# Kernel tuning notes

Measured on AMD Instinct MI355X. Metric: run time of the kernel, lower is better.

The kernel has to match this reference:

```python
import jax, jax.numpy as jnp
import numpy as np

B, T, N, H = 16, 49, 64, 128  # batch, input_window_size-1, nbones, hidden_size


def setup_inputs() -> dict:
    key = jax.random.key(0)
    ks = jax.random.split(key, 13)
    s = 0.1  # keep gate preactivations in a sane range
    inp = {
        "h": jax.random.normal(ks[0], (B, T, N, H), jnp.float32),
        "c_h": jax.random.normal(ks[1], (B, T, N, H), jnp.float32),
        "p": jax.random.normal(ks[2], (B, T, N, H), jnp.float32),
        "g_t": jax.random.normal(ks[3], (B, T, 1, H), jnp.float32),
        "c_g_t": jax.random.normal(ks[4], (B, T, 1, H), jnp.float32),
        # 8 h-update gates stacked: order = (i, f_lt, f_ft, f_rt, f_s, g, o, c)
        "U": jax.random.normal(ks[5], (8, T, H, H), jnp.float32) * s,     # acts on p
        "Wt": jax.random.normal(ks[6], (8, T, 3 * H, H), jnp.float32) * s,  # acts on [h_before,h,h_after]
        "Ws": jax.random.normal(ks[7], (8, T, H, H), jnp.float32) * s,    # acts on h_s_before
        "Zt": jax.random.normal(ks[8], (8, T, H, H), jnp.float32) * s,    # acts on g_t
        "b": jax.random.normal(ks[9], (8, T, 1, H), jnp.float32) * s,
        # 3 g_t-update gates stacked: order = (forget_f, g, o)
        "Wg": jax.random.normal(ks[10], (3, T, H, H), jnp.float32) * s,
        "Zg": jax.random.normal(ks[11], (3, T, H, H), jnp.float32) * s,
        "bg": jax.random.normal(ks[12], (3, T, 1, H), jnp.float32) * s,
        "train": 0,
    }
    return inp


def _forward(h, c_h, p, g_t, c_g_t, U, Wt, Ws, Zt, b, Wg, Zg, bg):
    zt = jnp.zeros_like(h[:, :1])        # temporal padding [B,1,N,H]
    zs = jnp.zeros_like(h[:, :, :1])     # spatial  padding [B,T,1,H]
    h_tb = jnp.concatenate([zt, h[:, :-1]], axis=1)
    h_ta = jnp.concatenate([h[:, 1:], zt], axis=1)
    h_tba = jnp.concatenate([h_tb, h, h_ta], axis=3)   # [B,T,N,3H]
    c_tb = jnp.concatenate([zt, c_h[:, :-1]], axis=1)
    c_ta = jnp.concatenate([c_h[:, 1:], zt], axis=1)
    h_sb = jnp.concatenate([zs, h[:, :, :-1]], axis=2)
    c_sb = jnp.concatenate([zs, c_h[:, :, :-1]], axis=2)

    # all 8 gate preactivations at once; per-timestep weights contracted with einsum
    pre = (jnp.einsum('btnh,gthk->gbtnk', p, U)
           + jnp.einsum('btnd,gtdk->gbtnk', h_tba, Wt)
           + jnp.einsum('btnh,gthk->gbtnk', h_sb, Ws)
           + jnp.einsum('btoh,gthk->gbtok', g_t, Zt)   # o == 1, broadcasts over bones
           + b[:, None])                               # [8,B,T,N,H]
    i_n, f_lt, f_ft, f_rt, f_s, g_n, o_n = jax.nn.sigmoid(pre[:7])
    c_n = jnp.tanh(pre[7])

    c_h_new = (i_n * c_n + f_lt * c_tb + f_ft * c_h + f_rt * c_ta
               + f_s * c_sb + g_n * c_g_t)
    h_new = o_n * jnp.tanh(c_h_new)

    # global (g_t) state update
    h_mean = jnp.mean(h_new, axis=2, keepdims=True)    # [B,T,1,H]
    f_gtf = jax.nn.sigmoid(jnp.einsum('btnh,thk->btnk', h_new, Wg[0])
                           + jnp.einsum('btoh,thk->btok', g_t, Zg[0]) + bg[0])
    g_gtg = jax.nn.sigmoid(jnp.einsum('btoh,thk->btok', h_mean, Wg[1])
                           + jnp.einsum('btoh,thk->btok', g_t, Zg[1]) + bg[1])
    o_gto = jax.nn.sigmoid(jnp.einsum('btoh,thk->btok', h_mean, Wg[2])
                           + jnp.einsum('btoh,thk->btok', g_t, Zg[2]) + bg[2])
    c_g_new = jnp.mean(f_gtf * c_h_new, axis=2, keepdims=True) + g_gtg * c_g_t
    g_new = jnp.tanh(c_g_new) * o_gto
    return h_new, c_h_new, g_new, c_g_new


def reference(h, c_h, p, g_t, c_g_t, U, Wt, Ws, Zt, b, Wg, Zg, bg, train):
    return _forward(h, c_h, p, g_t, c_g_t, U, Wt, Ws, Zt, b, Wg, Zg, bg)
```

## Files before the change

kernel.cpp:

```cpp
#include <hip/hip_runtime.h>
#include <hip/hip_bf16.h>

#define TD 49
#define BD 16
#define ND 64
#define HD 128

typedef float  f32x4  __attribute__((ext_vector_type(4)));
typedef __bf16 bf16x8 __attribute__((ext_vector_type(8)));
typedef __bf16 bf16x4 __attribute__((ext_vector_type(4)));

#define WP_OFF   0u
#define HB_OFF   38535168u
#define ACT_ELEMS 6422528u
#define PB_OFF   44957696u
#define GB_OFF   51380224u
#define GT_ELEMS 100352u
#define ZP_OFF   51480576u

#define OUT_H    0
#define OUT_CH   6422528
#define OUT_G    12845056
#define OUT_CG   12945408

#define KPAD 136
#define LDS1_BYTES 65536
#define LDS2_BYTES 118784

__device__ __forceinline__ float sigf(float x) {
    return 1.0f / (1.0f + exp2f(-1.442695041f * x));
}
__device__ __forceinline__ float tanhf_fast(float x) {
    x = fminf(fmaxf(x, -20.f), 20.f);
    float e = exp2f(2.885390082f * x);
    return (e - 1.f) / (e + 1.f);
}
__device__ __forceinline__ void gload16(const void* g, void* l) {
    __builtin_amdgcn_global_load_lds((const __attribute__((address_space(1))) void*)g,
                                     (__attribute__((address_space(3))) void*)l, 16, 0, 0);
}

__global__ void prep_acts(const float* __restrict__ h, const float* __restrict__ p,
                          const float* __restrict__ g, __bf16* __restrict__ ws)
{
    unsigned i = blockIdx.x * 256u + threadIdx.x;
    const unsigned HU = ACT_ELEMS / 4u, GU = GT_ELEMS / 4u;
    const float* src;
    unsigned dst;
    if (i < HU)                 { src = h + (size_t)i * 4;          dst = HB_OFF + i * 4; }
    else if (i < 2u*HU)         { unsigned j = i - HU;   src = p + (size_t)j * 4; dst = PB_OFF + j * 4; }
    else if (i < 2u*HU + GU)    { unsigned j = i - 2u*HU; src = g + (size_t)j * 4; dst = GB_OFF + j * 4; }
    else if (i < 2u*HU + GU + 512u) {
        unsigned j = i - 2u*HU - GU;
        bf16x4 z = {};
        *(bf16x4*)(ws + ZP_OFF + j * 4) = z;
        return;
    } else return;
    f32x4 v = *(const f32x4*)src;
    bf16x4 w;
    w[0] = (__bf16)v[0]; w[1] = (__bf16)v[1]; w[2] = (__bf16)v[2]; w[3] = (__bf16)v[3];
    *(bf16x4*)(ws + dst) = w;
}

__global__ __launch_bounds__(256) void prep_w(
    const float* __restrict__ U, const float* __restrict__ Wt,
    const float* __restrict__ Ws, const float* __restrict__ Zt,
    __bf16* __restrict__ wp)
{
    __shared__ __bf16 tile[64 * 132];
    int bid = blockIdx.x;
    int tg  = bid / 12;
    int c   = bid % 12;
    int t   = tg >> 3, g = tg & 7;
    int gt  = g * TD + t;
    int tid = threadIdx.x;
    int k0  = c * 64;

#pragma unroll
    for (int u = 0; u < 8; ++u) {
        int unit = u * 256 + tid;
        int kk = unit >> 5;
        int h4 = (unit & 31) << 2;
        int k  = k0 + kk;
        const float* src;
        if (k < 128)      src = U  + ((size_t)(gt * 128 + k)       << 7);
        else if (k < 512) src = Wt + ((size_t)(gt * 384 + (k-128)) << 7);
        else if (k < 640) src = Ws + ((size_t)(gt * 128 + (k-512)) << 7);
        else              src = Zt + ((size_t)(gt * 128 + (k-640)) << 7);
        f32x4 v = *(const f32x4*)(src + h4);
        bf16x4 w;
        w[0] = (__bf16)v[0]; w[1] = (__bf16)v[1]; w[2] = (__bf16)v[2]; w[3] = (__bf16)v[3];
        *(bf16x4*)(tile + kk * 132 + h4) = w;
    }
    __syncthreads();
#pragma unroll
    for (int u = 0; u < 2; ++u) {
        int unit = u * 256 + tid;
        int hh = unit >> 2;
        int kg = unit & 3;
        bf16x8 v0, v1;
#pragma unroll
        for (int j = 0; j < 8; ++j) v0[j] = tile[(kg * 16 + j) * 132 + hh];
#pragma unroll
        for (int j = 0; j < 8; ++j) v1[j] = tile[(kg * 16 + 8 + j) * 132 + hh];
        __bf16* dst = wp + (size_t)(tg * 128 + hh) * 768 + k0 + kg * 16;
        *(bf16x8*)dst       = v0;
        *(bf16x8*)(dst + 8) = v1;
    }
}

__global__ __launch_bounds__(256, 2) void phase1_kernel(
    const __bf16* __restrict__ ws,
    const float* __restrict__ c_h, const float* __restrict__ c_g_t,
    const float* __restrict__ bias, float* __restrict__ out)
{
    extern __shared__ __bf16 smem[];
    const __bf16* hb = ws + HB_OFF;
    const __bf16* pb = ws + PB_OFF;
    const __bf16* gb = ws + GB_OFF;
    const __bf16* wp = ws + WP_OFF;
    const __bf16* zp = ws + ZP_OFF;

    int bid = blockIdx.x;
    int swz = (bid & 7) * 392 + (bid >> 3);
    int t     = swz >> 6;
    int rem   = swz & 63;
    int mtile = rem >> 3, ntile = rem & 7;

    int tid  = threadIdx.x;
    int wave = tid >> 6, lane = tid & 63;
    int lg = lane >> 4, l16 = lane & 15;

    const __bf16* pA[2][6];
    const __bf16* pB[2];
    int dstA[2], dstB[2];
#pragma unroll
    for (int it = 0; it < 2; ++it) {
        int chunk = it * 256 + tid;
        int row   = chunk >> 2;
        int k16   = chunk & 3;
        int ke    = (k16 ^ ((row >> 1) & 3)) * 8;
        int b_ = mtile * 2 + (row >> 6), n_ = row & 63, bt_ = b_ * TD + t;
        pA[it][0] = pb + ((bt_ * ND + n_) << 7) + ke;
        pA[it][1] = (t > 0)      ? hb + (((bt_ - 1) * ND + n_) << 7) + ke : zp + ke;
        pA[it][2] = hb + ((bt_ * ND + n_) << 7) + ke;
        pA[it][3] = (t < TD - 1) ? hb + (((bt_ + 1) * ND + n_) << 7) + ke : zp + ke;
        pA[it][4] = (n_ > 0)     ? hb + ((bt_ * ND + n_ - 1) << 7) + ke : zp + ke;
        pA[it][5] = gb + (bt_ << 7) + ke;
        int g_ = row >> 4, hc = row & 15;
        pB[it] = wp + (size_t)((t * 8 + g_) * 128 + ntile * 16 + hc) * 768 + ke;
        dstA[it] = chunk * 8;
        dstB[it] = 16384 + chunk * 8;
    }

    int rbA[2], rbB[8];
#pragma unroll
    for (int mi = 0; mi < 2; ++mi) {
        int row = wave * 32 + mi * 16 + l16;
        rbA[mi] = row * 64 + ((lg ^ ((row >> 1) & 3)) << 4);
    }
#pragma unroll
    for (int g = 0; g < 8; ++g) {
        int row = g * 16 + l16;
        rbB[g] = 32768 + row * 64 + ((lg ^ ((row >> 1) & 3)) << 4);
    }

    f32x4 acc[2][8];
    const f32x4 vzero = {0.f, 0.f, 0.f, 0.f};
#pragma unroll
    for (int mi = 0; mi < 2; ++mi)
#pragma unroll
        for (int g = 0; g < 8; ++g) acc[mi][g] = vzero;

#define STAGE(KS) do {                                                          \
        _Pragma("unroll")                                                       \
        for (int it = 0; it < 2; ++it) {                                        \
            gload16(pA[it][(KS) >> 2] + ((KS) & 3) * 32,                        \
                    smem + ((KS) & 3) * 4096 + dstA[it]);                       \
            gload16(pB[it] + (KS) * 32,                                         \
                    smem + ((KS) & 3) * 4096 + dstB[it]);                       \
        }                                                                       \
    } while (0)

    STAGE(0); STAGE(1); STAGE(2);
    asm volatile("s_waitcnt vmcnt(8)" ::: "memory");
    __builtin_amdgcn_s_barrier();

#pragma unroll
    for (int ks = 0; ks < 24; ++ks) {
        if (ks + 3 < 24) STAGE(ks + 3);
        const char* base = (const char*)smem + (ks & 3) * 8192;
        bf16x8 af[2], bfr[8];
        af[0] = *(const bf16x8*)(base + rbA[0]);
        af[1] = *(const bf16x8*)(base + rbA[1]);
#pragma unroll
        for (int g = 0; g < 8; ++g)
            bfr[g] = *(const bf16x8*)(base + rbB[g]);
#pragma unroll
        for (int g = 0; g < 8; ++g) {
            acc[0][g] = __builtin_amdgcn_mfma_f32_16x16x32_bf16(af[0], bfr[g], acc[0][g], 0, 0, 0);
            acc[1][g] = __builtin_amdgcn_mfma_f32_16x16x32_bf16(af[1], bfr[g], acc[1][g], 0, 0, 0);
        }
        if (ks < 23) {
            if (ks < 21)       asm volatile("s_waitcnt vmcnt(8)" ::: "memory");
            else if (ks == 21) asm volatile("s_waitcnt vmcnt(4)" ::: "memory");
            else               asm volatile("s_waitcnt vmcnt(0)" ::: "memory");
            __builtin_amdgcn_s_barrier();
        }
    }
#undef STAGE

    const int hcol = ntile * 16 + l16;
    float bv[8];
#pragma unroll
    for (int g = 0; g < 8; ++g) bv[g] = bias[(g * TD + t) * HD + hcol];

#pragma unroll
    for (int mi = 0; mi < 2; ++mi) {
#pragma unroll
        for (int r = 0; r < 4; ++r) {
            int RG = mtile * 128 + wave * 32 + mi * 16 + lg * 4 + r;
            int b  = RG >> 6, nn = RG & 63;
            int bt = b * TD + t;
            int base = ((bt * ND + nn) << 7) + hcol;
            float pre[8];
#pragma unroll
            for (int g = 0; g < 8; ++g) pre[g] = acc[mi][g][r] + bv[g];
            float i_  = sigf(pre[0]);
            float flt = sigf(pre[1]);
            float fft = sigf(pre[2]);
            float frt = sigf(pre[3]);
            float fs  = sigf(pre[4]);
            float gn  = sigf(pre[5]);
            float on  = sigf(pre[6]);
            float cn  = tanhf_fast(pre[7]);
            float ccur = c_h[base];
            float ctb  = (t > 0)      ? c_h[base - ND * HD] : 0.f;
            float cta  = (t < TD - 1) ? c_h[base + ND * HD] : 0.f;
            float csb  = (nn > 0)     ? c_h[base - HD]      : 0.f;
            float cg   = c_g_t[(bt << 7) + hcol];
            float cnew = i_ * cn + flt * ctb + fft * ccur + frt * cta + fs * csb + gn * cg;
            float hnew = on * tanhf_fast(cnew);
            out[OUT_H  + base] = hnew;
            out[OUT_CH + base] = cnew;
        }
    }
}

__global__ __launch_bounds__(256, 1) void phase2_kernel(
    const float* __restrict__ g_t, const float* __restrict__ c_g_t,
    const float* __restrict__ Wg,  const float* __restrict__ Zg,
    const float* __restrict__ bg,  float* __restrict__ out)
{
    extern __shared__ char sm2[];
    __bf16* A2  = (__bf16*)sm2;
    __bf16* Wb  = (__bf16*)(sm2 + 69632);
    float*  gts = (float*)(sm2 + 69632 + 34816);
    float*  hm  = (float*)(sm2 + 69632 + 34816 + 2048);
    float*  dts = (float*)(sm2 + 69632 + 34816 + 4096);

    int bid = blockIdx.x;
    int t = bid >> 2, bq = bid & 3;
    int tid = threadIdx.x;
    int wv = tid >> 6, lane = tid & 63, lg = lane >> 4, l16 = lane & 15;

    const float* hn  = out + OUT_H;
    const float* chn = out + OUT_CH;

#pragma unroll
    for (int j = 0; j < 32; ++j) {
        int fid = j * 256 + tid;
        int r = fid >> 5, k = (fid & 31) << 2;
        int b = bq * 4 + (r >> 6), n = r & 63, bt = b * TD + t;
        f32x4 v = *(const f32x4*)(hn + ((bt * ND + n) << 7) + k);
        bf16x4 w;
        w[0] = (__bf16)v[0]; w[1] = (__bf16)v[1]; w[2] = (__bf16)v[2]; w[3] = (__bf16)v[3];
        *(bf16x4*)(A2 + r * KPAD + k) = w;
    }
#pragma unroll
    for (int j = 0; j < 2; ++j) {
        int idx = j * 256 + tid;
        int b4 = idx >> 7, c = idx & 127;
        gts[idx] = g_t[(((bq * 4 + b4) * TD + t) << 7) + c];
    }
    __syncthreads();

#pragma unroll
    for (int j = 0; j < 2; ++j) {
        int idx = j * 256 + tid;
        int b4 = idx >> 7, c = idx & 127;
        float s = 0.f;
        for (int n = 0; n < 64; ++n) s += (float)A2[(b4 * 64 + n) * KPAD + c];
        hm[idx] = s * (1.f / 64.f);
    }
    __syncthreads();

    for (int m = 0; m < 5; ++m) {
        const float* M = (m < 3) ? (Zg + ((size_t)(m * TD + t) << 14))
                                 : (Wg + ((size_t)((m - 2) * TD + t) << 14));
#pragma unroll
        for (int j = 0; j < 16; ++j) {
            int fid = j * 256 + tid;
            int k = fid >> 5, c4 = (fid & 31) << 2;
            f32x4 v = *(const f32x4*)(M + (k << 7) + c4);
            bf16x4 w;
            w[0] = (__bf16)v[0]; w[1] = (__bf16)v[1]; w[2] = (__bf16)v[2]; w[3] = (__bf16)v[3];
            *(bf16x4*)(Wb + k * KPAD + c4) = w;
        }
        __syncthreads();
        const float* vec = (m >= 3) ? hm : gts;
#pragma unroll
        for (int j = 0; j < 2; ++j) {
            int idx = j * 256 + tid;
            int b4 = idx >> 7, c = idx & 127;
            float s = 0.f;
            for (int k = 0; k < 128; ++k) s += vec[b4 * 128 + k] * (float)Wb[k * KPAD + c];
            dts[(m * 4 + b4) * 128 + c] = s;
        }
        __syncthreads();
    }

    {
        const float* M = Wg + ((size_t)t << 14);
#pragma unroll
        for (int j = 0; j < 16; ++j) {
            int fid = j * 256 + tid;
            int k = fid >> 5, q = fid & 31;
            f32x4 v = *(const f32x4*)(M + (k << 7) + q * 4);
            int cb = q * 4;
            Wb[(cb + 0) * KPAD + k] = (__bf16)v[0];
            Wb[(cb + 1) * KPAD + k] = (__bf16)v[1];
            Wb[(cb + 2) * KPAD + k] = (__bf16)v[2];
            Wb[(cb + 3) * KPAD + k] = (__bf16)v[3];
        }
        __syncthreads();
    }

    f32x4 acc[4][8];
    const f32x4 vzero = {0.f, 0.f, 0.f, 0.f};
#pragma unroll
    for (int mi = 0; mi < 4; ++mi)
#pragma unroll
        for (int ni = 0; ni < 8; ++ni) acc[mi][ni] = vzero;
#pragma unroll
    for (int ks = 0; ks < 4; ++ks) {
        int kb = ks * 32 + lg * 8;
        bf16x8 a[4];
#pragma unroll
        for (int mi = 0; mi < 4; ++mi)
            a[mi] = *(const bf16x8*)(A2 + (wv * 64 + mi * 16 + l16) * KPAD + kb);
#pragma unroll
        for (int ni = 0; ni < 8; ++ni) {
            bf16x8 bfr = *(const bf16x8*)(Wb + (ni * 16 + l16) * KPAD + kb);
#pragma unroll
            for (int mi = 0; mi < 4; ++mi)
                acc[mi][ni] = __builtin_amdgcn_mfma_f32_16x16x32_bf16(a[mi], bfr, acc[mi][ni], 0, 0, 0);
        }
    }

    int b = bq * 4 + wv, bt = b * TD + t;
#pragma unroll
    for (int ni = 0; ni < 8; ++ni) {
        int col = ni * 16 + l16;
        float z = dts[(0 * 4 + wv) * 128 + col] + bg[t * HD + col];
        float macc = 0.f;
#pragma unroll
        for (int mi = 0; mi < 4; ++mi) {
#pragma unroll
            for (int r = 0; r < 4; ++r) {
                int row = mi * 16 + lg * 4 + r;
                float f  = sigf(acc[mi][ni][r] + z);
                float cv = chn[((bt * ND + row) << 7) + col];
                macc += f * cv;
            }
        }
        macc += __shfl_xor(macc, 16, 64);
        macc += __shfl_xor(macc, 32, 64);
        if (lg == 0) {
            float Mn  = macc * (1.f / 64.f);
            float g_g = sigf(dts[(3 * 4 + wv) * 128 + col] + dts[(1 * 4 + wv) * 128 + col]
                             + bg[(TD + t) * HD + col]);
            float o_g = sigf(dts[(4 * 4 + wv) * 128 + col] + dts[(2 * 4 + wv) * 128 + col]
                             + bg[(2 * TD + t) * HD + col]);
            float cgt = c_g_t[(bt << 7) + col];
            float cgn = Mn + g_g * cgt;
            out[OUT_G  + (bt << 7) + col] = tanhf_fast(cgn) * o_g;
            out[OUT_CG + (bt << 7) + col] = cgn;
        }
    }
}

extern "C" void kernel_launch(void* const* d_in, const int* in_sizes, int n_in,
                              void* d_out, int out_size, void* d_ws, size_t ws_size,
                              hipStream_t stream) {
    const float* h     = (const float*)d_in[0];
    const float* c_h   = (const float*)d_in[1];
    const float* p     = (const float*)d_in[2];
    const float* g_t   = (const float*)d_in[3];
    const float* c_g_t = (const float*)d_in[4];
    const float* U     = (const float*)d_in[5];
    const float* Wt    = (const float*)d_in[6];
    const float* Ws    = (const float*)d_in[7];
    const float* Zt    = (const float*)d_in[8];
    const float* b     = (const float*)d_in[9];
    const float* Wg    = (const float*)d_in[10];
    const float* Zg    = (const float*)d_in[11];
    const float* bg    = (const float*)d_in[12];
    float* out = (float*)d_out;
    __bf16* ws = (__bf16*)d_ws;

    prep_acts<<<12644, 256, 0, stream>>>(h, p, g_t, ws);
    prep_w<<<TD * 8 * 12, 256, 0, stream>>>(U, Wt, Ws, Zt, ws + WP_OFF);

    (void)hipFuncSetAttribute(reinterpret_cast<const void*>(phase1_kernel),
                              hipFuncAttributeMaxDynamicSharedMemorySize, LDS1_BYTES);
    (void)hipFuncSetAttribute(reinterpret_cast<const void*>(phase2_kernel),
                              hipFuncAttributeMaxDynamicSharedMemorySize, LDS2_BYTES);
    phase1_kernel<<<TD * 64, 256, LDS1_BYTES, stream>>>(ws, c_h, c_g_t, b, out);
    phase2_kernel<<<TD * 4, 256, LDS2_BYTES, stream>>>(g_t, c_g_t, Wg, Zg, bg, out);
}
```

Baseline: 234.9 us.

## Double phase1 M-tile to 256 rows with 3-stage LDS pipeline

Phase1 now computes a 256x128 output tile per block instead of 128x128, so each B-weight fragment read from LDS feeds four MFMAs rather than two, and half as many blocks are launched. The LDS ring shrinks from four stages to three with separate A and B regions, and address computation switches to 32-bit offsets. This roughly halves redundant weight traffic per output, at the cost of twice the accumulator registers (which may lower occupancy) and fewer blocks to spread across CUs.

Result: slower. 282.4 us (+20.2%).

```diff
diff --git a/kernel.cpp b/kernel.cpp
--- a/kernel.cpp
+++ b/kernel.cpp
@@ -24,7 +24,7 @@
 #define OUT_CG   12945408
 
 #define KPAD 136
-#define LDS1_BYTES 65536
+#define LDS1_BYTES 73728
 #define LDS2_BYTES 118784
 
 __device__ __forceinline__ float sigf(float x) {
@@ -115,96 +115,100 @@
     const float* __restrict__ bias, float* __restrict__ out)
 {
     extern __shared__ __bf16 smem[];
-    const __bf16* hb = ws + HB_OFF;
-    const __bf16* pb = ws + PB_OFF;
-    const __bf16* gb = ws + GB_OFF;
-    const __bf16* wp = ws + WP_OFF;
-    const __bf16* zp = ws + ZP_OFF;
 
     int bid = blockIdx.x;
-    int swz = (bid & 7) * 392 + (bid >> 3);
-    int t     = swz >> 6;
-    int rem   = swz & 63;
+    int swz = (bid & 7) * 196 + (bid >> 3);
+    int t     = swz >> 5;
+    int rem   = swz & 31;
     int mtile = rem >> 3, ntile = rem & 7;
 
     int tid  = threadIdx.x;
     int wave = tid >> 6, lane = tid & 63;
     int lg = lane >> 4, l16 = lane & 15;
 
-    const __bf16* pA[2][6];
-    const __bf16* pB[2];
-    int dstA[2], dstB[2];
+    const int n    = tid >> 2;
+    const unsigned kesw = (((tid & 3) ^ ((tid >> 3) & 3)) << 3);
+    const bool okT0 = (t > 0), okT1 = (t < TD - 1), okN = (n > 0);
+    const unsigned zoff = ZP_OFF + kesw;
+    const int tid8 = tid * 8;
+
+    unsigned rowoff[4], goff[4], offB[2];
+#pragma unroll
+    for (int it = 0; it < 4; ++it) {
+        unsigned bt_ = (unsigned)((mtile * 4 + it) * TD + t);
+        rowoff[it] = bt_ * 8192u + (unsigned)(n << 7) + kesw;
+        goff[it]   = bt_ * 128u + kesw;
+    }
 #pragma unroll
     for (int it = 0; it < 2; ++it) {
-        int chunk = it * 256 + tid;
-        int row   = chunk >> 2;
-        int k16   = chunk & 3;
-        int ke    = (k16 ^ ((row >> 1) & 3)) * 8;
-        int b_ = mtile * 2 + (row >> 6), n_ = row & 63, bt_ = b_ * TD + t;
-        pA[it][0] = pb + ((bt_ * ND + n_) << 7) + ke;
-        pA[it][1] = (t > 0)      ? hb + (((bt_ - 1) * ND + n_) << 7) + ke : zp + ke;
-        pA[it][2] = hb + ((bt_ * ND + n_) << 7) + ke;
-        pA[it][3] = (t < TD - 1) ? hb + (((bt_ + 1) * ND + n_) << 7) + ke : zp + ke;
-        pA[it][4] = (n_ > 0)     ? hb + ((bt_ * ND + n_ - 1) << 7) + ke : zp + ke;
-        pA[it][5] = gb + (bt_ << 7) + ke;
+        int row = it * 64 + n;
         int g_ = row >> 4, hc = row & 15;
-        pB[it] = wp + (size_t)((t * 8 + g_) * 128 + ntile * 16 + hc) * 768 + ke;
-        dstA[it] = chunk * 8;
-        dstB[it] = 16384 + chunk * 8;
-    }
-
-    int rbA[2], rbB[8];
-#pragma unroll
-    for (int mi = 0; mi < 2; ++mi) {
-        int row = wave * 32 + mi * 16 + l16;
+        offB[it] = WP_OFF + (unsigned)((t * 8 + g_) * 128 + ntile * 16 + hc) * 768u + kesw;
+    }
+
+    f32x4 acc[4][8];
+    const f32x4 vzero = {0.f, 0.f, 0.f, 0.f};
+#pragma unroll
+    for (int mi = 0; mi < 4; ++mi)
+#pragma unroll
+        for (int g = 0; g < 8; ++g) acc[mi][g] = vzero;
+
+    int rbA[4], rbB[8];
+#pragma unroll
+    for (int mi = 0; mi < 4; ++mi) {
+        int row = wave * 64 + mi * 16 + l16;
         rbA[mi] = row * 64 + ((lg ^ ((row >> 1) & 3)) << 4);
     }
 #pragma unroll
     for (int g = 0; g < 8; ++g) {
         int row = g * 16 + l16;
-        rbB[g] = 32768 + row * 64 + ((lg ^ ((row >> 1) & 3)) << 4);
-    }
-
-    f32x4 acc[2][8];
-    const f32x4 vzero = {0.f, 0.f, 0.f, 0.f};
-#pragma unroll
-    for (int mi = 0; mi < 2; ++mi)
-#pragma unroll
-        for (int g = 0; g < 8; ++g) acc[mi][g] = vzero;
+        rbB[g] = row * 64 + ((lg ^ ((row >> 1) & 3)) << 4);
+    }
 
 #define STAGE(KS) do {                                                          \
+        const int s_ = (KS) >> 2;                                               \
+        const int sl = (KS) % 3;                                                \
         _Pragma("unroll")                                                       \
-        for (int it = 0; it < 2; ++it) {                                        \
-            gload16(pA[it][(KS) >> 2] + ((KS) & 3) * 32,                        \
-                    smem + ((KS) & 3) * 4096 + dstA[it]);                       \
-            gload16(pB[it] + (KS) * 32,                                         \
-                    smem + ((KS) & 3) * 4096 + dstB[it]);                       \
+        for (int it = 0; it < 4; ++it) {                                        \
+            unsigned off;                                                       \
+            if (s_ == 0)      off = PB_OFF + rowoff[it];                        \
+            else if (s_ == 1) off = okT0 ? HB_OFF + rowoff[it] - 8192u : zoff;  \
+            else if (s_ == 2) off = HB_OFF + rowoff[it];                        \
+            else if (s_ == 3) off = okT1 ? HB_OFF + rowoff[it] + 8192u : zoff;  \
+            else if (s_ == 4) off = okN  ? HB_OFF + rowoff[it] - 128u  : zoff;  \
+            else              off = GB_OFF + goff[it];                          \
+            gload16(ws + off + ((KS) & 3) * 32, smem + sl * 8192 + tid8 + it * 2048); \
         }                                                                       \
+        _Pragma("unroll")                                                       \
+        for (int it = 0; it < 2; ++it)                                          \
+            gload16(ws + offB[it] + (KS) * 32,                                  \
+                    smem + 24576 + sl * 4096 + tid8 + it * 2048);               \
     } while (0)
 
-    STAGE(0); STAGE(1); STAGE(2);
-    asm volatile("s_waitcnt vmcnt(8)" ::: "memory");
+    STAGE(0); STAGE(1);
+    asm volatile("s_waitcnt vmcnt(6)" ::: "memory");
     __builtin_amdgcn_s_barrier();
 
 #pragma unroll
     for (int ks = 0; ks < 24; ++ks) {
-        if (ks + 3 < 24) STAGE(ks + 3);
-        const char* base = (const char*)smem + (ks & 3) * 8192;
-        bf16x8 af[2], bfr[8];
-        af[0] = *(const bf16x8*)(base + rbA[0]);
-        af[1] = *(const bf16x8*)(base + rbA[1]);
+        if (ks + 2 < 24) STAGE(ks + 2);
+        const char* Ab = (const char*)smem + (ks % 3) * 16384;
+        const char* Bb = (const char*)smem + 49152 + (ks % 3) * 8192;
+        bf16x8 af[4], bfr[8];
+#pragma unroll
+        for (int mi = 0; mi < 4; ++mi)
+            af[mi] = *(const bf16x8*)(Ab + rbA[mi]);
 #pragma unroll
         for (int g = 0; g < 8; ++g)
-            bfr[g] = *(const bf16x8*)(base + rbB[g]);
-#pragma unroll
-        for (int g = 0; g < 8; ++g) {
-            acc[0][g] = __builtin_amdgcn_mfma_f32_16x16x32_bf16(af[0], bfr[g], acc[0][g], 0, 0, 0);
-            acc[1][g] = __builtin_amdgcn_mfma_f32_16x16x32_bf16(af[1], bfr[g], acc[1][g], 0, 0, 0);
-        }
+            bfr[g] = *(const bf16x8*)(Bb + rbB[g]);
+#pragma unroll
+        for (int g = 0; g < 8; ++g)
+#pragma unroll
+            for (int mi = 0; mi < 4; ++mi)
+                acc[mi][g] = __builtin_amdgcn_mfma_f32_16x16x32_bf16(af[mi], bfr[g], acc[mi][g], 0, 0, 0);
         if (ks < 23) {
-            if (ks < 21)       asm volatile("s_waitcnt vmcnt(8)" ::: "memory");
-            else if (ks == 21) asm volatile("s_waitcnt vmcnt(4)" ::: "memory");
-            else               asm volatile("s_waitcnt vmcnt(0)" ::: "memory");
+            if (ks < 22) asm volatile("s_waitcnt vmcnt(6)" ::: "memory");
+            else         asm volatile("s_waitcnt vmcnt(0)" ::: "memory");
             __builtin_amdgcn_s_barrier();
         }
     }
@@ -216,10 +220,10 @@
     for (int g = 0; g < 8; ++g) bv[g] = bias[(g * TD + t) * HD + hcol];
 
 #pragma unroll
-    for (int mi = 0; mi < 2; ++mi) {
+    for (int mi = 0; mi < 4; ++mi) {
 #pragma unroll
         for (int r = 0; r < 4; ++r) {
-            int RG = mtile * 128 + wave * 32 + mi * 16 + lg * 4 + r;
+            int RG = mtile * 256 + wave * 64 + mi * 16 + lg * 4 + r;
             int b  = RG >> 6, nn = RG & 63;
             int bt = b * TD + t;
             int base = ((bt * ND + nn) << 7) + hcol;
@@ -271,8 +275,8 @@
     for (int j = 0; j < 32; ++j) {
         int fid = j * 256 + tid;
         int r = fid >> 5, k = (fid & 31) << 2;
-        int b = bq * 4 + (r >> 6), n = r & 63, bt = b * TD + t;
-        f32x4 v = *(const f32x4*)(hn + ((bt * ND + n) << 7) + k);
+        int b = bq * 4 + (r >> 6), nn = r & 63, bt = b * TD + t;
+        f32x4 v = *(const f32x4*)(hn + ((bt * ND + nn) << 7) + k);
         bf16x4 w;
         w[0] = (__bf16)v[0]; w[1] = (__bf16)v[1]; w[2] = (__bf16)v[2]; w[3] = (__bf16)v[3];
         *(bf16x4*)(A2 + r * KPAD + k) = w;
@@ -290,7 +294,7 @@
         int idx = j * 256 + tid;
         int b4 = idx >> 7, c = idx & 127;
         float s = 0.f;
-        for (int n = 0; n < 64; ++n) s += (float)A2[(b4 * 64 + n) * KPAD + c];
+        for (int nn = 0; nn < 64; ++nn) s += (float)A2[(b4 * 64 + nn) * KPAD + c];
         hm[idx] = s * (1.f / 64.f);
     }
     __syncthreads();
@@ -416,6 +420,6 @@
                               hipFuncAttributeMaxDynamicSharedMemorySize, LDS1_BYTES);
     (void)hipFuncSetAttribute(reinterpret_cast<const void*>(phase2_kernel),
                               hipFuncAttributeMaxDynamicSharedMemorySize, LDS2_BYTES);
-    phase1_kernel<<<TD * 64, 256, LDS1_BYTES, stream>>>(ws, c_h, c_g_t, b, out);
+    phase1_kernel<<<TD * 32, 256, LDS1_BYTES, stream>>>(ws, c_h, c_g_t, b, out);
     phase2_kernel<<<TD * 4, 256, LDS2_BYTES, stream>>>(g_t, c_g_t, Wg, Zg, bg, out);
 }
```

## Precompute g_t·Zt plus bias per (b,t) and drop Zt from main GEMM

Applied to the files above, without the earlier changes.

The g_t term is constant across the 64 bones, so its projection through Zt plus the bias is precomputed once per (batch, timestep, gate) in a new prep block group and added in the epilogue. The main MFMA GEMM K dimension shrinks from 768 to 640, cutting weight packing, loads and MFMA work by about a sixth. The two prep kernels are also merged into one launch. The trade-off is an extra fp32 scalar prep stage and per-element gathered loads of the precomputed term in the phase1 epilogue.

After: 282.2 us. 1.2x slower.

```diff
diff --git a/kernel.cpp b/kernel.cpp
--- a/kernel.cpp
+++ b/kernel.cpp
@@ -11,12 +11,13 @@
 typedef __bf16 bf16x4 __attribute__((ext_vector_type(4)));
 
 #define WP_OFF   0u
-#define HB_OFF   38535168u
+#define HB_OFF   32112640u
 #define ACT_ELEMS 6422528u
-#define PB_OFF   44957696u
-#define GB_OFF   51380224u
+#define PB_OFF   38535168u
+#define GB_OFF   44957696u
 #define GT_ELEMS 100352u
-#define ZP_OFF   51480576u
+#define ZP_OFF   45058048u
+#define ZB_OFF   45060096u
 
 #define OUT_H    0
 #define OUT_CH   6422528
@@ -27,6 +28,10 @@
 #define LDS1_BYTES 65536
 #define LDS2_BYTES 118784
 
+#define NB_ACTS 12644
+#define NB_W    3920
+#define NB_ZB   392
+
 __device__ __forceinline__ float sigf(float x) {
     return 1.0f / (1.0f + exp2f(-1.442695041f * x));
 }
@@ -40,86 +45,112 @@
                                      (__attribute__((address_space(3))) void*)l, 16, 0, 0);
 }
 
-__global__ void prep_acts(const float* __restrict__ h, const float* __restrict__ p,
-                          const float* __restrict__ g, __bf16* __restrict__ ws)
-{
-    unsigned i = blockIdx.x * 256u + threadIdx.x;
-    const unsigned HU = ACT_ELEMS / 4u, GU = GT_ELEMS / 4u;
-    const float* src;
-    unsigned dst;
-    if (i < HU)                 { src = h + (size_t)i * 4;          dst = HB_OFF + i * 4; }
-    else if (i < 2u*HU)         { unsigned j = i - HU;   src = p + (size_t)j * 4; dst = PB_OFF + j * 4; }
-    else if (i < 2u*HU + GU)    { unsigned j = i - 2u*HU; src = g + (size_t)j * 4; dst = GB_OFF + j * 4; }
-    else if (i < 2u*HU + GU + 512u) {
-        unsigned j = i - 2u*HU - GU;
-        bf16x4 z = {};
-        *(bf16x4*)(ws + ZP_OFF + j * 4) = z;
-        return;
-    } else return;
-    f32x4 v = *(const f32x4*)src;
-    bf16x4 w;
-    w[0] = (__bf16)v[0]; w[1] = (__bf16)v[1]; w[2] = (__bf16)v[2]; w[3] = (__bf16)v[3];
-    *(bf16x4*)(ws + dst) = w;
-}
-
-__global__ __launch_bounds__(256) void prep_w(
-    const float* __restrict__ U, const float* __restrict__ Wt,
-    const float* __restrict__ Ws, const float* __restrict__ Zt,
-    __bf16* __restrict__ wp)
+__global__ __launch_bounds__(256) void prep_kernel(
+    const float* __restrict__ h,  const float* __restrict__ p,
+    const float* __restrict__ g,  const float* __restrict__ U,
+    const float* __restrict__ Wt, const float* __restrict__ Ws,
+    const float* __restrict__ Zt, const float* __restrict__ bias,
+    __bf16* __restrict__ ws)
 {
     __shared__ __bf16 tile[64 * 132];
-    int bid = blockIdx.x;
-    int tg  = bid / 12;
-    int c   = bid % 12;
-    int t   = tg >> 3, g = tg & 7;
-    int gt  = g * TD + t;
-    int tid = threadIdx.x;
-    int k0  = c * 64;
-
-#pragma unroll
-    for (int u = 0; u < 8; ++u) {
-        int unit = u * 256 + tid;
-        int kk = unit >> 5;
-        int h4 = (unit & 31) << 2;
-        int k  = k0 + kk;
+    const int bid = blockIdx.x;
+    const int tid = threadIdx.x;
+
+    if (bid < NB_ACTS) {
+        unsigned i = bid * 256u + tid;
+        const unsigned HU = ACT_ELEMS / 4u, GU = GT_ELEMS / 4u;
         const float* src;
-        if (k < 128)      src = U  + ((size_t)(gt * 128 + k)       << 7);
-        else if (k < 512) src = Wt + ((size_t)(gt * 384 + (k-128)) << 7);
-        else if (k < 640) src = Ws + ((size_t)(gt * 128 + (k-512)) << 7);
-        else              src = Zt + ((size_t)(gt * 128 + (k-640)) << 7);
-        f32x4 v = *(const f32x4*)(src + h4);
+        unsigned dst;
+        if (i < HU)              { src = h + (size_t)i * 4;            dst = HB_OFF + i * 4; }
+        else if (i < 2u*HU)      { unsigned j = i - HU;    src = p + (size_t)j * 4; dst = PB_OFF + j * 4; }
+        else if (i < 2u*HU + GU) { unsigned j = i - 2u*HU; src = g + (size_t)j * 4; dst = GB_OFF + j * 4; }
+        else if (i < 2u*HU + GU + 512u) {
+            unsigned j = i - 2u*HU - GU;
+            bf16x4 z = {};
+            *(bf16x4*)(ws + ZP_OFF + j * 4) = z;
+            return;
+        } else return;
+        f32x4 v = *(const f32x4*)src;
         bf16x4 w;
         w[0] = (__bf16)v[0]; w[1] = (__bf16)v[1]; w[2] = (__bf16)v[2]; w[3] = (__bf16)v[3];
-        *(bf16x4*)(tile + kk * 132 + h4) = w;
-    }
-    __syncthreads();
-#pragma unroll
-    for (int u = 0; u < 2; ++u) {
-        int unit = u * 256 + tid;
-        int hh = unit >> 2;
-        int kg = unit & 3;
-        bf16x8 v0, v1;
-#pragma unroll
-        for (int j = 0; j < 8; ++j) v0[j] = tile[(kg * 16 + j) * 132 + hh];
-#pragma unroll
-        for (int j = 0; j < 8; ++j) v1[j] = tile[(kg * 16 + 8 + j) * 132 + hh];
-        __bf16* dst = wp + (size_t)(tg * 128 + hh) * 768 + k0 + kg * 16;
-        *(bf16x8*)dst       = v0;
-        *(bf16x8*)(dst + 8) = v1;
+        *(bf16x4*)(ws + dst) = w;
+        return;
+    }
+
+    if (bid < NB_ACTS + NB_W) {
+        int wb = bid - NB_ACTS;
+        int tg = wb / 10, c = wb % 10;
+        int t  = tg >> 3, gg = tg & 7;
+        int gt = gg * TD + t;
+        int k0 = c * 64;
+#pragma unroll
+        for (int u = 0; u < 8; ++u) {
+            int unit = u * 256 + tid;
+            int kk = unit >> 5;
+            int h4 = (unit & 31) << 2;
+            int k  = k0 + kk;
+            const float* src;
+            if (k < 128)      src = U  + ((size_t)(gt * 128 + k)       << 7);
+            else if (k < 512) src = Wt + ((size_t)(gt * 384 + (k-128)) << 7);
+            else              src = Ws + ((size_t)(gt * 128 + (k-512)) << 7);
+            f32x4 v = *(const f32x4*)(src + h4);
+            bf16x4 w;
+            w[0] = (__bf16)v[0]; w[1] = (__bf16)v[1]; w[2] = (__bf16)v[2]; w[3] = (__bf16)v[3];
+            *(bf16x4*)(tile + kk * 132 + h4) = w;
+        }
+        __syncthreads();
+#pragma unroll
+        for (int u = 0; u < 2; ++u) {
+            int unit = u * 256 + tid;
+            int hh = unit >> 2;
+            int kg = unit & 3;
+            bf16x8 v0, v1;
+#pragma unroll
+            for (int j = 0; j < 8; ++j) v0[j] = tile[(kg * 16 + j) * 132 + hh];
+#pragma unroll
+            for (int j = 0; j < 8; ++j) v1[j] = tile[(kg * 16 + 8 + j) * 132 + hh];
+            __bf16* dst = ws + WP_OFF + (size_t)(tg * 128 + hh) * 640 + k0 + kg * 16;
+            *(bf16x8*)dst       = v0;
+            *(bf16x8*)(dst + 8) = v1;
+        }
+        return;
+    }
+
+    {
+        int zid = bid - NB_ACTS - NB_W;
+        int t = zid >> 3, gg = zid & 7;
+        int h_ = tid & 127, bh = tid >> 7;
+        float* zbf = (float*)(ws + ZB_OFF);
+        float s[8];
+        float bv = bias[(gg * TD + t) * HD + h_];
+#pragma unroll
+        for (int b8 = 0; b8 < 8; ++b8) s[b8] = bv;
+        const float* Zrow = Zt + ((size_t)(gg * TD + t) << 14) + h_;
+        for (int k = 0; k < 128; ++k) {
+            float zv = Zrow[k << 7];
+#pragma unroll
+            for (int b8 = 0; b8 < 8; ++b8)
+                s[b8] += g[(((bh * 8 + b8) * TD + t) << 7) + k] * zv;
+        }
+#pragma unroll
+        for (int b8 = 0; b8 < 8; ++b8) {
+            int bt = (bh * 8 + b8) * TD + t;
+            zbf[(bt * 8 + gg) * HD + h_] = s[b8];
+        }
     }
 }
 
 __global__ __launch_bounds__(256, 2) void phase1_kernel(
     const __bf16* __restrict__ ws,
     const float* __restrict__ c_h, const float* __restrict__ c_g_t,
-    const float* __restrict__ bias, float* __restrict__ out)
+    float* __restrict__ out)
 {
     extern __shared__ __bf16 smem[];
     const __bf16* hb = ws + HB_OFF;
     const __bf16* pb = ws + PB_OFF;
-    const __bf16* gb = ws + GB_OFF;
     const __bf16* wp = ws + WP_OFF;
     const __bf16* zp = ws + ZP_OFF;
+    const float*  zb = (const float*)(ws + ZB_OFF);
 
     int bid = blockIdx.x;
     int swz = (bid & 7) * 392 + (bid >> 3);
@@ -131,7 +162,7 @@
     int wave = tid >> 6, lane = tid & 63;
     int lg = lane >> 4, l16 = lane & 15;
 
-    const __bf16* pA[2][6];
+    const __bf16* pA[2][5];
     const __bf16* pB[2];
     int dstA[2], dstB[2];
 #pragma unroll
@@ -146,9 +177,8 @@
         pA[it][2] = hb + ((bt_ * ND + n_) << 7) + ke;
         pA[it][3] = (t < TD - 1) ? hb + (((bt_ + 1) * ND + n_) << 7) + ke : zp + ke;
         pA[it][4] = (n_ > 0)     ? hb + ((bt_ * ND + n_ - 1) << 7) + ke : zp + ke;
-        pA[it][5] = gb + (bt_ << 7) + ke;
         int g_ = row >> 4, hc = row & 15;
-        pB[it] = wp + (size_t)((t * 8 + g_) * 128 + ntile * 16 + hc) * 768 + ke;
+        pB[it] = wp + (size_t)((t * 8 + g_) * 128 + ntile * 16 + hc) * 640 + ke;
         dstA[it] = chunk * 8;
         dstB[it] = 16384 + chunk * 8;
     }
@@ -187,8 +217,8 @@
     __builtin_amdgcn_s_barrier();
 
 #pragma unroll
-    for (int ks = 0; ks < 24; ++ks) {
-        if (ks + 3 < 24) STAGE(ks + 3);
+    for (int ks = 0; ks < 20; ++ks) {
+        if (ks + 3 < 20) STAGE(ks + 3);
         const char* base = (const char*)smem + (ks & 3) * 8192;
         bf16x8 af[2], bfr[8];
         af[0] = *(const bf16x8*)(base + rbA[0]);
@@ -201,9 +231,9 @@
             acc[0][g] = __builtin_amdgcn_mfma_f32_16x16x32_bf16(af[0], bfr[g], acc[0][g], 0, 0, 0);
             acc[1][g] = __builtin_amdgcn_mfma_f32_16x16x32_bf16(af[1], bfr[g], acc[1][g], 0, 0, 0);
         }
-        if (ks < 23) {
-            if (ks < 21)       asm volatile("s_waitcnt vmcnt(8)" ::: "memory");
-            else if (ks == 21) asm volatile("s_waitcnt vmcnt(4)" ::: "memory");
+        if (ks < 19) {
+            if (ks < 17)       asm volatile("s_waitcnt vmcnt(8)" ::: "memory");
+            else if (ks == 17) asm volatile("s_waitcnt vmcnt(4)" ::: "memory");
             else               asm volatile("s_waitcnt vmcnt(0)" ::: "memory");
             __builtin_amdgcn_s_barrier();
         }
@@ -211,10 +241,6 @@
 #undef STAGE
 
     const int hcol = ntile * 16 + l16;
-    float bv[8];
-#pragma unroll
-    for (int g = 0; g < 8; ++g) bv[g] = bias[(g * TD + t) * HD + hcol];
-
 #pragma unroll
     for (int mi = 0; mi < 2; ++mi) {
 #pragma unroll
@@ -223,9 +249,10 @@
             int b  = RG >> 6, nn = RG & 63;
             int bt = b * TD + t;
             int base = ((bt * ND + nn) << 7) + hcol;
+            const float* zrow = zb + (bt * 8) * HD + hcol;
             float pre[8];
 #pragma unroll
-            for (int g = 0; g < 8; ++g) pre[g] = acc[mi][g][r] + bv[g];
+            for (int g = 0; g < 8; ++g) pre[g] = acc[mi][g][r] + zrow[g * HD];
             float i_  = sigf(pre[0]);
             float flt = sigf(pre[1]);
             float fft = sigf(pre[2]);
@@ -271,8 +298,8 @@
     for (int j = 0; j < 32; ++j) {
         int fid = j * 256 + tid;
         int r = fid >> 5, k = (fid & 31) << 2;
-        int b = bq * 4 + (r >> 6), n = r & 63, bt = b * TD + t;
-        f32x4 v = *(const f32x4*)(hn + ((bt * ND + n) << 7) + k);
+        int b = bq * 4 + (r >> 6), nn = r & 63, bt = b * TD + t;
+        f32x4 v = *(const f32x4*)(hn + ((bt * ND + nn) << 7) + k);
         bf16x4 w;
         w[0] = (__bf16)v[0]; w[1] = (__bf16)v[1]; w[2] = (__bf16)v[2]; w[3] = (__bf16)v[3];
         *(bf16x4*)(A2 + r * KPAD + k) = w;
@@ -290,7 +317,7 @@
         int idx = j * 256 + tid;
         int b4 = idx >> 7, c = idx & 127;
         float s = 0.f;
-        for (int n = 0; n < 64; ++n) s += (float)A2[(b4 * 64 + n) * KPAD + c];
+        for (int nn = 0; nn < 64; ++nn) s += (float)A2[(b4 * 64 + nn) * KPAD + c];
         hm[idx] = s * (1.f / 64.f);
     }
     __syncthreads();
@@ -409,13 +436,12 @@
     float* out = (float*)d_out;
     __bf16* ws = (__bf16*)d_ws;
 
-    prep_acts<<<12644, 256, 0, stream>>>(h, p, g_t, ws);
-    prep_w<<<TD * 8 * 12, 256, 0, stream>>>(U, Wt, Ws, Zt, ws + WP_OFF);
+    prep_kernel<<<NB_ACTS + NB_W + NB_ZB, 256, 0, stream>>>(h, p, g_t, U, Wt, Ws, Zt, b, ws);
 
     (void)hipFuncSetAttribute(reinterpret_cast<const void*>(phase1_kernel),
                               hipFuncAttributeMaxDynamicSharedMemorySize, LDS1_BYTES);
     (void)hipFuncSetAttribute(reinterpret_cast<const void*>(phase2_kernel),
                               hipFuncAttributeMaxDynamicSharedMemorySize, LDS2_BYTES);
-    phase1_kernel<<<TD * 64, 256, LDS1_BYTES, stream>>>(ws, c_h, c_g_t, b, out);
+    phase1_kernel<<<TD * 64, 256, LDS1_BYTES, stream>>>(ws, c_h, c_g_t, out);
     phase2_kernel<<<TD * 4, 256, LDS2_BYTES, stream>>>(g_t, c_g_t, Wg, Zg, bg, out);
 }
```
